# Performance work log

Hardware: AMD Instinct MI355X
Metric: run time of the kernel (lower is better)

The kernel has to match this reference:

```python
import jax, jax.numpy as jnp
import numpy as np

B, H, W, C = 16, 56, 56, 256
NH, WS, SS = 8, 7, 3          # heads, window size, shift size
HD = C // NH                  # head dim = 32
MLPD = 4 * C                  # mlp hidden = 1024
WA = WS * WS                  # window area = 49
NW = (H // WS) * (W // WS)    # windows per image = 64
SCALE = HD ** -0.5


def _rel_pos_index():
    coords = np.stack(np.meshgrid(np.arange(WS), np.arange(WS), indexing='ij'))
    cf = coords.reshape(2, -1)
    rel = (cf[:, :, None] - cf[:, None, :]).transpose(1, 2, 0)
    rel[:, :, 0] += WS - 1
    rel[:, :, 1] += WS - 1
    rel[:, :, 0] *= 2 * WS - 1
    return rel.sum(-1)  # (WA, WA) int


def _shift_attn_mask():
    img = np.zeros((H, W))
    cnt = 0
    for hs in (slice(0, -WS), slice(-WS, -SS), slice(-SS, None)):
        for ws_ in (slice(0, -WS), slice(-WS, -SS), slice(-SS, None)):
            img[hs, ws_] = cnt
            cnt += 1
    mw = img.reshape(H // WS, WS, W // WS, WS).transpose(0, 2, 1, 3).reshape(-1, WA)
    am = mw[:, None, :] - mw[:, :, None]
    return np.where(am != 0, -100.0, 0.0).astype(np.float32)  # (NW, WA, WA)

REL_IDX = jnp.asarray(_rel_pos_index())
ATTN_MASK = jnp.asarray(_shift_attn_mask())


def setup_inputs() -> dict:
    key = jax.random.key(0)
    ks = jax.random.split(key, 8)
    s = 0.02
    return {
        'x':      jax.random.normal(ks[0], (B, H * W, C), jnp.float32),
        'g1':     jnp.ones((C,), jnp.float32),
        'be1':    jnp.zeros((C,), jnp.float32),
        'w_qkv':  jax.random.normal(ks[1], (C, 3 * C), jnp.float32) * s,
        'b_qkv':  jnp.zeros((3 * C,), jnp.float32),
        'rpt':    jax.random.normal(ks[2], ((2 * WS - 1) ** 2, NH), jnp.float32) * s,
        'w_proj': jax.random.normal(ks[3], (C, C), jnp.float32) * s,
        'b_proj': jnp.zeros((C,), jnp.float32),
        'g2':     jnp.ones((C,), jnp.float32),
        'be2':    jnp.zeros((C,), jnp.float32),
        'w_fc1':  jax.random.normal(ks[4], (C, MLPD), jnp.float32) * s,
        'b_fc1':  jnp.zeros((MLPD,), jnp.float32),
        'w_fc2':  jax.random.normal(ks[5], (MLPD, C), jnp.float32) * s,
        'b_fc2':  jnp.zeros((C,), jnp.float32),
    }


def _ln(x, g, b, eps=1e-5):
    m = x.mean(-1, keepdims=True)
    v = ((x - m) ** 2).mean(-1, keepdims=True)
    return (x - m) * jax.lax.rsqrt(v + eps) * g + b


def reference(x, g1, be1, w_qkv, b_qkv, rpt, w_proj, b_proj, g2, be2,
              w_fc1, b_fc1, w_fc2, b_fc2):
    shortcut = x
    h = _ln(x, g1, be1).reshape(B, H, W, C)
    # cyclic shift
    h = jnp.roll(h, (-SS, -SS), axis=(1, 2))
    # window partition -> (B*NW, WA, C)
    h = h.reshape(B, H // WS, WS, W // WS, WS, C).transpose(0, 1, 3, 2, 4, 5)
    h = h.reshape(B * NW, WA, C)
    # qkv
    qkv = h @ w_qkv + b_qkv                       # (B*NW, WA, 3C)
    qkv = qkv.reshape(B * NW, WA, 3, NH, HD).transpose(2, 0, 3, 1, 4)
    q, k, v = qkv[0], qkv[1], qkv[2]              # (B*NW, NH, WA, HD)
    attn = jnp.einsum('wnqd,wnkd->wnqk', q * SCALE, k)   # (B*NW, NH, WA, WA)
    # relative position bias
    bias = rpt[REL_IDX.reshape(-1)].reshape(WA, WA, NH).transpose(2, 0, 1)
    attn = attn + bias[None]
    # shifted-window mask, per window
    attn = attn.reshape(B, NW, NH, WA, WA) + ATTN_MASK[None, :, None]
    attn = jax.nn.softmax(attn.reshape(B * NW, NH, WA, WA), axis=-1)
    out = jnp.einsum('wnqk,wnkd->wnqd', attn, v)  # (B*NW, NH, WA, HD)
    out = out.transpose(0, 2, 1, 3).reshape(B * NW, WA, C)
    out = out @ w_proj + b_proj
    # window reverse + unshift
    out = out.reshape(B, H // WS, W // WS, WS, WS, C).transpose(0, 1, 3, 2, 4, 5)
    out = out.reshape(B, H, W, C)
    out = jnp.roll(out, (SS, SS), axis=(1, 2)).reshape(B, H * W, C)
    x = shortcut + out
    # MLP block
    h2 = _ln(x, g2, be2)
    h2 = jax.nn.gelu(h2 @ w_fc1 + b_fc1, approximate=False) @ w_fc2 + b_fc2
    return x + h2
```

## Files before the change

### kernel.cpp

```cpp
#include <hip/hip_runtime.h>
#include <hip/hip_bf16.h>
#include <cstdint>
#include <cstddef>
#include <type_traits>

typedef __attribute__((ext_vector_type(8))) short short8;
typedef __attribute__((ext_vector_type(4))) float f32x4;
typedef __attribute__((ext_vector_type(4))) unsigned short us4;

#define DEVINL __device__ __forceinline__

static constexpr int SS_ = 3;
static constexpr int HH = 56, WW = 56;
#define SCALE_Q 0.17677669529663689f

DEVINL unsigned short f2b(float f) {
    unsigned int u = __builtin_bit_cast(unsigned int, f);
    unsigned int r = (u + 0x7FFFu + ((u >> 16) & 1u)) >> 16;
    return (unsigned short)r;
}
DEVINL float b2f(unsigned short s) {
    return __builtin_bit_cast(float, ((unsigned int)s) << 16);
}

DEVINL float gelu(float v) {
    float ax = fabsf(v) * 0.70710678118654752f;
    float t = 1.0f / (1.0f + 0.47047f * ax);
    float poly = t * (0.3480242f + t * (-0.0958798f + t * 0.7478556f));
    float erfv = 1.0f - poly * __expf(-ax * ax);
    erfv = v >= 0.0f ? erfv : -erfv;
    return 0.5f * v * (1.0f + erfv);
}

DEVINL void gload_lds16(const unsigned short* g, unsigned short* l) {
    __builtin_amdgcn_global_load_lds(
        (const __attribute__((address_space(1))) unsigned int*)g,
        (__attribute__((address_space(3))) unsigned int*)l, 16, 0, 0);
}

__global__ void wconv4_kernel(const float* __restrict__ w0,
                              const float* __restrict__ w1,
                              const float* __restrict__ w2,
                              const float* __restrict__ w3,
                              unsigned short* __restrict__ o0,
                              unsigned short* __restrict__ o1,
                              unsigned short* __restrict__ o2,
                              unsigned short* __restrict__ o3) {
    int b = blockIdx.x;
    const float* in; unsigned short* out; int K, N, base;
    if (b < 768)       { in = w0; out = o0; K = 256;  N = 768;  base = 0; }
    else if (b < 1024) { in = w1; out = o1; K = 256;  N = 256;  base = 768; }
    else if (b < 2048) { in = w2; out = o2; K = 256;  N = 1024; base = 1024; }
    else               { in = w3; out = o3; K = 1024; N = 256;  base = 2048; }
    int i = (b - base) * 256 + threadIdx.x;
    int k = i / N, n = i - k * N;
    out[(size_t)n * K + k] = f2b(in[i]);
}

template <int MODE, typename TIN>
__global__ __launch_bounds__(256) void ln_kernel(
    const TIN* __restrict__ x, const float* __restrict__ g,
    const float* __restrict__ be, unsigned short* __restrict__ out) {
    const int wid = threadIdx.x >> 6, lane = threadIdx.x & 63;
    const int t = blockIdx.x * 4 + wid;
    int src;
    if constexpr (MODE == 1) {
        int w = t / 49, p = t - w * 49;
        int b = w >> 6, widx = w & 63;
        int wy = widx >> 3, wx = widx & 7;
        int py = p / 7, px = p - py * 7;
        int y = wy * 7 + py + SS_;  if (y >= HH) y -= HH;
        int xx = wx * 7 + px + SS_; if (xx >= WW) xx -= WW;
        src = b * (HH * WW) + y * WW + xx;
    } else {
        src = t;
    }
    float4 v;
    if constexpr (std::is_same_v<TIN, float>) {
        v = reinterpret_cast<const float4*>(x + (size_t)src * 256)[lane];
    } else {
        us4 u = reinterpret_cast<const us4*>(x + (size_t)src * 256)[lane];
        v.x = b2f(u.x); v.y = b2f(u.y); v.z = b2f(u.z); v.w = b2f(u.w);
    }
    float s = v.x + v.y + v.z + v.w;
    float q = v.x * v.x + v.y * v.y + v.z * v.z + v.w * v.w;
#pragma unroll
    for (int m = 1; m < 64; m <<= 1) {
        s += __shfl_xor(s, m);
        q += __shfl_xor(q, m);
    }
    float mean = s * (1.0f / 256.0f);
    float var = q * (1.0f / 256.0f) - mean * mean;
    float rs = rsqrtf(var + 1e-5f);
    int c = lane * 4;
    us4 o;
    o.x = f2b((v.x - mean) * rs * g[c + 0] + be[c + 0]);
    o.y = f2b((v.y - mean) * rs * g[c + 1] + be[c + 1]);
    o.z = f2b((v.z - mean) * rs * g[c + 2] + be[c + 2]);
    o.w = f2b((v.w - mean) * rs * g[c + 3] + be[c + 3]);
    *reinterpret_cast<us4*>(out + (size_t)t * 256 + c) = o;
}

template <int KDIM, int EPI>
__global__ __launch_bounds__(256, 4) void gemm_kernel(
    const unsigned short* __restrict__ A, const unsigned short* __restrict__ Bt,
    const float* __restrict__ bias, void* __restrict__ out0,
    const void* __restrict__ res, unsigned short* __restrict__ o_q,
    unsigned short* __restrict__ o_k, unsigned short* __restrict__ o_v) {
    constexpr int BM = 128, BN = 128, BK = 64;
    __shared__ __align__(16) unsigned short As[BM * BK];
    __shared__ __align__(16) unsigned short Bs[BN * BK];
    const int tid = threadIdx.x;
    const int wid = tid >> 6, lane = tid & 63;

    const int nwg = gridDim.x * gridDim.y;
    const int bid = blockIdx.x + gridDim.x * blockIdx.y;
    const int nb = (bid & 7) * (nwg >> 3) + (bid >> 3);
    const int n0 = (nb % gridDim.x) * BN;
    const int m0 = (nb / gridDim.x) * BM;

    const int wm = wid >> 1, wn = wid & 1;
    const int lr = lane & 15, kg = lane >> 4;
    f32x4 acc[4][4] = {};

    const int srow = tid >> 3;
    const int spos = tid & 7;

    for (int kt = 0; kt < KDIM; kt += BK) {
#pragma unroll
        for (int i = 0; i < 4; i++) {
            int row = i * 32 + srow;
            gload_lds16(A + (size_t)(m0 + row) * KDIM + kt + ((spos ^ (row & 7)) << 3),
                        As + i * 2048 + tid * 8);
        }
#pragma unroll
        for (int i = 0; i < 4; i++) {
            int row = i * 32 + srow;
            gload_lds16(Bt + (size_t)(n0 + row) * KDIM + kt + ((spos ^ (row & 7)) << 3),
                        Bs + i * 2048 + tid * 8);
        }
        __syncthreads();
#pragma unroll
        for (int ks = 0; ks < 2; ks++) {
            short8 a[4], b[4];
#pragma unroll
            for (int mf = 0; mf < 4; mf++) {
                int r = wm * 64 + mf * 16 + lr;
                a[mf] = *reinterpret_cast<const short8*>(
                    As + r * 64 + (((ks * 4 + kg) ^ (r & 7)) << 3));
            }
#pragma unroll
            for (int nf = 0; nf < 4; nf++) {
                int r = wn * 64 + nf * 16 + lr;
                b[nf] = *reinterpret_cast<const short8*>(
                    Bs + r * 64 + (((ks * 4 + kg) ^ (r & 7)) << 3));
            }
#pragma unroll
            for (int mf = 0; mf < 4; mf++)
#pragma unroll
                for (int nf = 0; nf < 4; nf++)
                    acc[mf][nf] = __builtin_amdgcn_mfma_f32_16x16x32_bf16(
                        a[mf], b[nf], acc[mf][nf], 0, 0, 0);
        }
        __syncthreads();
    }

#pragma unroll
    for (int mf = 0; mf < 4; mf++) {
#pragma unroll
        for (int nf = 0; nf < 4; nf++) {
#pragma unroll
            for (int j = 0; j < 4; j++) {
                int row = m0 + wm * 64 + mf * 16 + kg * 4 + j;
                int col = n0 + wn * 64 + nf * 16 + lr;
                float v = acc[mf][nf][j] + bias[col];
                if constexpr (EPI == 0) {
                    int w = row / 49, p = row - w * 49;
                    int which = col >> 8, h = (col >> 5) & 7, d = col & 31;
                    size_t th = (size_t)(w * 8 + h);
                    if (which == 0)
                        o_q[th * 1568 + p * 32 + d] = f2b(v * SCALE_Q);
                    else if (which == 1)
                        o_k[th * 1568 + p * 32 + d] = f2b(v);
                    else
                        o_v[th * 1568 + p * 32 + d] = f2b(v);
                } else if constexpr (EPI == 1) {
                    int w = row / 49, p = row - w * 49;
                    int b2 = w >> 6, widx = w & 63;
                    int wy = widx >> 3, wx = widx & 7;
                    int py = p / 7, px = p - py * 7;
                    int y = wy * 7 + py + SS_;  if (y >= HH) y -= HH;
                    int xx = wx * 7 + px + SS_; if (xx >= WW) xx -= WW;
                    size_t oi = ((size_t)(b2 * 3136 + y * 56 + xx)) * 256 + col;
                    reinterpret_cast<unsigned short*>(out0)[oi] =
                        f2b(v + reinterpret_cast<const float*>(res)[oi]);
                } else if constexpr (EPI == 2) {
                    reinterpret_cast<unsigned short*>(out0)[(size_t)row * 1024 + col] =
                        f2b(gelu(v));
                } else {
                    size_t oi = (size_t)row * 256 + col;
                    reinterpret_cast<float*>(out0)[oi] =
                        v + b2f(reinterpret_cast<const unsigned short*>(res)[oi]);
                }
            }
        }
    }
}

__global__ __launch_bounds__(256) void attn_kernel(
    const unsigned short* __restrict__ qg, const unsigned short* __restrict__ kgl,
    const unsigned short* __restrict__ vg, const float* __restrict__ rpt,
    unsigned short* __restrict__ out) {
    __shared__ __align__(16) unsigned short sm[4][6144];
    __shared__ unsigned short rpts[169 * 8];
    const int tid = threadIdx.x, wid = tid >> 6, lane = tid & 63;
    for (int i = tid; i < 169 * 8; i += 256) rpts[i] = f2b(rpt[i]);
    const int task = blockIdx.x * 4 + wid;
    const int w = task >> 3, h = task & 7;
    const int widx = w & 63, wy = widx >> 3, wx = widx & 7;
    unsigned short* q_s = sm[wid];
    unsigned short* k_s = sm[wid] + 2048;
    unsigned short* v_s = sm[wid] + 4096;
    unsigned short* p_s = sm[wid];
    const unsigned short* qsrc = qg + (size_t)task * 1568;
    const unsigned short* ksrc = kgl + (size_t)task * 1568;
    const unsigned short* vsrc = vg + (size_t)task * 1568;
    for (int i = lane; i < 512; i += 64) {
        int d = i >> 4, p = 48 + (i & 15);
        v_s[d * 64 + (p ^ ((d & 7) << 3))] = 0;
    }
    for (int c = lane; c < 196; c += 64) {
        int row = c >> 2, kc = c & 3;
        int off = (row * 32 + kc * 8) ^ ((row & 7) << 3);
        *reinterpret_cast<short8*>(q_s + off) =
            *reinterpret_cast<const short8*>(qsrc + c * 8);
        *reinterpret_cast<short8*>(k_s + off) =
            *reinterpret_cast<const short8*>(ksrc + c * 8);
        short8 vv = *reinterpret_cast<const short8*>(vsrc + c * 8);
        int p = c >> 2, d0 = (c & 3) * 8;
#pragma unroll
        for (int e = 0; e < 8; e++) {
            int d = d0 + e;
            v_s[d * 64 + (p ^ ((d & 7) << 3))] = (unsigned short)vv[e];
        }
    }
    __syncthreads();

    const int lr = lane & 15, kg = lane >> 4;
    short8 af[4], bf[4];
#pragma unroll
    for (int mf = 0; mf < 4; mf++) {
        int r = mf * 16 + lr;
        af[mf] = *reinterpret_cast<const short8*>(
            q_s + ((r * 32 + kg * 8) ^ ((r & 7) << 3)));
    }
#pragma unroll
    for (int nf = 0; nf < 4; nf++) {
        int r = nf * 16 + lr;
        bf[nf] = *reinterpret_cast<const short8*>(
            k_s + ((r * 32 + kg * 8) ^ ((r & 7) << 3)));
    }
    f32x4 s[4][4] = {};
#pragma unroll
    for (int mf = 0; mf < 4; mf++)
#pragma unroll
        for (int nf = 0; nf < 4; nf++)
            s[mf][nf] = __builtin_amdgcn_mfma_f32_16x16x32_bf16(af[mf], bf[nf],
                                                                s[mf][nf], 0, 0, 0);
#pragma unroll
    for (int mf = 0; mf < 4; mf++) {
#pragma unroll
        for (int j = 0; j < 4; j++) {
            int row = mf * 16 + kg * 4 + j;
            bool rvalid = row < 49;
            int qy = 0, qx = 0, gq = 0;
            if (rvalid) {
                qy = row / 7; qx = row - qy * 7;
                int yi = wy * 7 + qy, xi = wx * 7 + qx;
                gq = ((yi < 49) ? 0 : ((yi < 53) ? 1 : 2)) * 3 +
                     ((xi < 49) ? 0 : ((xi < 53) ? 1 : 2));
            }
            float L[4];
#pragma unroll
            for (int nf = 0; nf < 4; nf++) {
                int col = nf * 16 + lr;
                float val = s[mf][nf][j];
                if (rvalid && col < 49) {
                    int ky = col / 7, kx = col - ky * 7;
                    int yi = wy * 7 + ky, xi = wx * 7 + kx;
                    int gk = ((yi < 49) ? 0 : ((yi < 53) ? 1 : 2)) * 3 +
                             ((xi < 49) ? 0 : ((xi < 53) ? 1 : 2));
                    val += b2f(rpts[((qy - ky + 6) * 13 + (qx - kx + 6)) * 8 + h]);
                    if (gq != gk) val -= 100.0f;
                } else {
                    val = -1e30f;
                }
                L[nf] = val;
            }
            float m = fmaxf(fmaxf(L[0], L[1]), fmaxf(L[2], L[3]));
#pragma unroll
            for (int t2 = 1; t2 < 16; t2 <<= 1) m = fmaxf(m, __shfl_xor(m, t2));
            float P[4], psum = 0.f;
#pragma unroll
            for (int nf = 0; nf < 4; nf++) {
                P[nf] = __expf(L[nf] - m);
                psum += P[nf];
            }
#pragma unroll
            for (int t2 = 1; t2 < 16; t2 <<= 1) psum += __shfl_xor(psum, t2);
            float inv = 1.0f / psum;
#pragma unroll
            for (int nf = 0; nf < 4; nf++) {
                int col = nf * 16 + lr;
                p_s[(row * 64 + col) ^ ((row & 7) << 3)] = f2b(P[nf] * inv);
            }
        }
    }
    f32x4 o[4][2] = {};
#pragma unroll
    for (int ks = 0; ks < 2; ks++) {
        short8 pa[4], vb[2];
#pragma unroll
        for (int mf = 0; mf < 4; mf++) {
            int r = mf * 16 + lr;
            pa[mf] = *reinterpret_cast<const short8*>(
                p_s + ((r * 64 + ks * 32 + kg * 8) ^ ((r & 7) << 3)));
        }
#pragma unroll
        for (int nf = 0; nf < 2; nf++) {
            int d = nf * 16 + lr;
            vb[nf] = *reinterpret_cast<const short8*>(
                v_s + ((d * 64 + ks * 32 + kg * 8) ^ ((d & 7) << 3)));
        }
#pragma unroll
        for (int mf = 0; mf < 4; mf++)
#pragma unroll
            for (int nf = 0; nf < 2; nf++)
                o[mf][nf] = __builtin_amdgcn_mfma_f32_16x16x32_bf16(
                    pa[mf], vb[nf], o[mf][nf], 0, 0, 0);
    }
#pragma unroll
    for (int mf = 0; mf < 4; mf++) {
#pragma unroll
        for (int j = 0; j < 4; j++) {
            int row = mf * 16 + kg * 4 + j;
            if (row < 49) {
#pragma unroll
                for (int nf = 0; nf < 2; nf++) {
                    int d = nf * 16 + lr;
                    out[((size_t)w * 49 + row) * 256 + h * 32 + d] =
                        f2b(o[mf][nf][j]);
                }
            }
        }
    }
}

extern "C" void kernel_launch(void* const* d_in, const int* in_sizes, int n_in,
                              void* d_out, int out_size, void* d_ws,
                              size_t ws_size, hipStream_t stream) {
    const float* x     = (const float*)d_in[0];
    const float* g1    = (const float*)d_in[1];
    const float* be1   = (const float*)d_in[2];
    const float* wqkv  = (const float*)d_in[3];
    const float* bqkv  = (const float*)d_in[4];
    const float* rpt   = (const float*)d_in[5];
    const float* wproj = (const float*)d_in[6];
    const float* bproj = (const float*)d_in[7];
    const float* g2    = (const float*)d_in[8];
    const float* be2   = (const float*)d_in[9];
    const float* wfc1  = (const float*)d_in[10];
    const float* bfc1  = (const float*)d_in[11];
    const float* wfc2  = (const float*)d_in[12];
    const float* bfc2  = (const float*)d_in[13];
    float* out = (float*)d_out;
    char* ws = (char*)d_ws;

    unsigned short* hb  = (unsigned short*)(ws);
    unsigned short* qg  = (unsigned short*)(ws + 25690112);
    unsigned short* kgl = (unsigned short*)(ws + 51380224);
    unsigned short* vg  = (unsigned short*)(ws + 77070336);
    unsigned short* x2b = (unsigned short*)(ws + 110624768);
    unsigned short* h2  = (unsigned short*)(ws + 162004992);
    unsigned short* wT  = (unsigned short*)(ws + 187695104);
    unsigned short* wqkvT = wT;
    unsigned short* wprojT = wT + 196608;
    unsigned short* wfc1T  = wT + 262144;
    unsigned short* wfc2T  = wT + 524288;
    unsigned short* a1 = (unsigned short*)ws;

    wconv4_kernel<<<3072, 256, 0, stream>>>(wqkv, wproj, wfc1, wfc2,
                                            wqkvT, wprojT, wfc1T, wfc2T);

    ln_kernel<1, float><<<12544, 256, 0, stream>>>(x, g1, be1, hb);
    gemm_kernel<256, 0><<<dim3(6, 392), 256, 0, stream>>>(
        hb, wqkvT, bqkv, nullptr, nullptr, qg, kgl, vg);
    attn_kernel<<<2048, 256, 0, stream>>>(qg, kgl, vg, rpt, hb);
    gemm_kernel<256, 1><<<dim3(2, 392), 256, 0, stream>>>(
        hb, wprojT, bproj, x2b, x, nullptr, nullptr, nullptr);
    ln_kernel<0, unsigned short><<<12544, 256, 0, stream>>>(x2b, g2, be2, h2);
    gemm_kernel<256, 2><<<dim3(8, 392), 256, 0, stream>>>(
        h2, wfc1T, bfc1, a1, nullptr, nullptr, nullptr, nullptr);
    gemm_kernel<1024, 3><<<dim3(2, 392), 256, 0, stream>>>(
        a1, wfc2T, bfc2, out, x2b, nullptr, nullptr, nullptr);
}
```

Baseline: 257.3 us.

## Double-buffer GEMM shared-memory tiles with BK=32 to overlap loads and MFMA

The GEMM kernel now uses two LDS buffers of BK=32 instead of one BK=64 buffer. The next k-tile is prefetched asynchronously while MFMAs run on the current tile, leaving one barrier per iteration instead of two. The XOR swizzle is adjusted to 4 slots per row. This is meant to hide global-to-LDS latency, at the cost of more loop iterations with less MFMA work each, and possibly more LDS bank conflicts from the narrower swizzle.

```diff
diff --git a/kernel.cpp b/kernel.cpp
--- a/kernel.cpp
+++ b/kernel.cpp
@@ -107,9 +107,9 @@
     const float* __restrict__ bias, void* __restrict__ out0,
     const void* __restrict__ res, unsigned short* __restrict__ o_q,
     unsigned short* __restrict__ o_k, unsigned short* __restrict__ o_v) {
-    constexpr int BM = 128, BN = 128, BK = 64;
-    __shared__ __align__(16) unsigned short As[BM * BK];
-    __shared__ __align__(16) unsigned short Bs[BN * BK];
+    constexpr int BM = 128, BN = 128, BK = 32, NK = KDIM / BK;
+    __shared__ __align__(16) unsigned short As[2][BM * BK];
+    __shared__ __align__(16) unsigned short Bs[2][BN * BK];
     const int tid = threadIdx.x;
     const int wid = tid >> 6, lane = tid & 63;
 
@@ -123,46 +123,52 @@
     const int lr = lane & 15, kg = lane >> 4;
     f32x4 acc[4][4] = {};
 
-    const int srow = tid >> 3;
-    const int spos = tid & 7;
-
-    for (int kt = 0; kt < KDIM; kt += BK) {
-#pragma unroll
-        for (int i = 0; i < 4; i++) {
-            int row = i * 32 + srow;
-            gload_lds16(A + (size_t)(m0 + row) * KDIM + kt + ((spos ^ (row & 7)) << 3),
-                        As + i * 2048 + tid * 8);
-        }
-#pragma unroll
-        for (int i = 0; i < 4; i++) {
-            int row = i * 32 + srow;
-            gload_lds16(Bt + (size_t)(n0 + row) * KDIM + kt + ((spos ^ (row & 7)) << 3),
-                        Bs + i * 2048 + tid * 8);
-        }
+    const int srow = tid >> 2;
+    const int sslot = tid & 3;
+
+    auto STAGE = [&](int kt, int buf) {
+#pragma unroll
+        for (int i = 0; i < 2; i++) {
+            int row = i * 64 + srow;
+            gload_lds16(A + (size_t)(m0 + row) * KDIM + kt * BK +
+                            ((sslot ^ (row & 3)) << 3),
+                        As[buf] + i * 2048 + tid * 8);
+        }
+#pragma unroll
+        for (int i = 0; i < 2; i++) {
+            int row = i * 64 + srow;
+            gload_lds16(Bt + (size_t)(n0 + row) * KDIM + kt * BK +
+                            ((sslot ^ (row & 3)) << 3),
+                        Bs[buf] + i * 2048 + tid * 8);
+        }
+    };
+
+    STAGE(0, 0);
+    __syncthreads();
+    int cur = 0;
+    for (int kt = 0; kt < NK; kt++) {
+        if (kt + 1 < NK) STAGE(kt + 1, cur ^ 1);
+        short8 a[4], b[4];
+#pragma unroll
+        for (int mf = 0; mf < 4; mf++) {
+            int r = wm * 64 + mf * 16 + lr;
+            a[mf] = *reinterpret_cast<const short8*>(
+                As[cur] + r * 32 + ((kg ^ (r & 3)) << 3));
+        }
+#pragma unroll
+        for (int nf = 0; nf < 4; nf++) {
+            int r = wn * 64 + nf * 16 + lr;
+            b[nf] = *reinterpret_cast<const short8*>(
+                Bs[cur] + r * 32 + ((kg ^ (r & 3)) << 3));
+        }
+#pragma unroll
+        for (int mf = 0; mf < 4; mf++)
+#pragma unroll
+            for (int nf = 0; nf < 4; nf++)
+                acc[mf][nf] = __builtin_amdgcn_mfma_f32_16x16x32_bf16(
+                    a[mf], b[nf], acc[mf][nf], 0, 0, 0);
         __syncthreads();
-#pragma unroll
-        for (int ks = 0; ks < 2; ks++) {
-            short8 a[4], b[4];
-#pragma unroll
-            for (int mf = 0; mf < 4; mf++) {
-                int r = wm * 64 + mf * 16 + lr;
-                a[mf] = *reinterpret_cast<const short8*>(
-                    As + r * 64 + (((ks * 4 + kg) ^ (r & 7)) << 3));
-            }
-#pragma unroll
-            for (int nf = 0; nf < 4; nf++) {
-                int r = wn * 64 + nf * 16 + lr;
-                b[nf] = *reinterpret_cast<const short8*>(
-                    Bs + r * 64 + (((ks * 4 + kg) ^ (r & 7)) << 3));
-            }
-#pragma unroll
-            for (int mf = 0; mf < 4; mf++)
-#pragma unroll
-                for (int nf = 0; nf < 4; nf++)
-                    acc[mf][nf] = __builtin_amdgcn_mfma_f32_16x16x32_bf16(
-                        a[mf], b[nf], acc[mf][nf], 0, 0, 0);
-        }
-        __syncthreads();
+        cur ^= 1;
     }
 
 #pragma unroll
```

Result: slower. 272.0 us (+5.7%).
